# Performance work log

Measured on AMD Instinct MI355X. Metric: run time of the kernel, lower is better.

## Reference

```python
import jax, jax.numpy as jnp
import numpy as np

B, T, E, H = 4, 2048, 512, 8
D = E // H  # head_dim = 64


def setup_inputs() -> dict:
    key = jax.random.key(0)
    ks = jax.random.split(key, 9)
    s = 1.0 / np.sqrt(E)
    inp = {
        "x": jax.random.normal(ks[0], (B, T, E), dtype=jnp.float32),
        "Wq": jax.random.normal(ks[1], (E, E), dtype=jnp.float32) * s,
        "bq": jnp.zeros((E,), dtype=jnp.float32),
        "Wk": jax.random.normal(ks[2], (E, E), dtype=jnp.float32) * s,
        "bk": jnp.zeros((E,), dtype=jnp.float32),
        "Wv": jax.random.normal(ks[3], (E, E), dtype=jnp.float32) * s,
        "bv": jnp.zeros((E,), dtype=jnp.float32),
        "Wo": jax.random.normal(ks[4], (E, E), dtype=jnp.float32) * s,
        "bo": jnp.zeros((E,), dtype=jnp.float32),
    }
    return inp


def reference(x, Wq, bq, Wk, bk, Wv, bv, Wo, bo):
    # x: (B, T, E); weights stored (in, out) so y = x @ W + b
    b, t, _ = x.shape
    q = (x @ Wq + bq).reshape(b, t, H, D).transpose(0, 2, 1, 3)  # (B,H,T,D)
    k = (x @ Wk + bk).reshape(b, t, H, D).transpose(0, 2, 1, 3)  # (B,H,T,D)
    v = (x @ Wv + bv).reshape(b, t, H, D).transpose(0, 2, 1, 3)  # (B,H,T,D)
    scores = jnp.einsum("bhqd,bhkd->bhqk", q, k) / np.sqrt(D)    # (B,H,Tq,Tk)
    # faithful to source: softmax over dim=-2 (the query axis)
    attn = jax.nn.softmax(scores, axis=-2)
    out = jnp.einsum("bhqk,bhkd->bhqd", attn, v)                  # (B,H,T,D)
    # faithful to source: reshape (B,H,T,D) -> (B,T,H*D) with NO transpose
    out = out.reshape(b, t, H * D)
    return out @ Wo + bo
```

## Files before the change

### kernel.cpp

```cpp
#include <hip/hip_runtime.h>
#include <hip/hip_bf16.h>

#define NB 4
#define NT 2048
#define NE 512
#define NH 8
#define ND 64
#define BH (NB*NH)

typedef __attribute__((ext_vector_type(8))) short short8;
typedef __attribute__((ext_vector_type(4))) short short4v;
typedef __attribute__((ext_vector_type(4))) float f32x4;

typedef const __attribute__((address_space(3))) short* lds_sp;

__device__ __forceinline__ f32x4 mfma16(short8 a, short8 b, f32x4 c){
  return __builtin_amdgcn_mfma_f32_16x16x32_bf16(a, b, c, 0, 0, 0);
}
__device__ __forceinline__ short f2b(float f){
  union { float f; unsigned u; } v; v.f = f;
  unsigned r = v.u + 0x7FFFu + ((v.u >> 16) & 1u);
  return (short)(r >> 16);
}
__device__ __forceinline__ float b2f(short s){
  union { unsigned u; float f; } v; v.u = ((unsigned)(unsigned short)s) << 16; return v.f;
}
__device__ __forceinline__ unsigned pk2(float a, float b){
  union { __hip_bfloat162 h; unsigned u; } v;
  v.h = __float22bfloat162_rn(make_float2(a, b));
  return v.u;
}
__device__ __forceinline__ void gld16(const void* g, void* l){
  __builtin_amdgcn_global_load_lds((const __attribute__((address_space(1))) void*)g,
                                   (__attribute__((address_space(3))) void*)l, 16, 0, 0);
}
__device__ __forceinline__ short4v trr(lds_sp p, int imm){
  short4v r;
  asm volatile("ds_read_b64_tr_b16 %0, %1 offset:%2" : "=v"(r) : "v"(p), "i"(imm));
  return r;
}

__global__ __launch_bounds__(256) void pack_x_k(const float* __restrict__ x, short* __restrict__ xb){
  int i = blockIdx.x*256 + threadIdx.x;
  f32x4 a = ((const f32x4*)x)[2*i];
  f32x4 b = ((const f32x4*)x)[2*i+1];
  union { short8 s; unsigned u[4]; } o;
  o.u[0] = pk2(a[0], a[1]);
  o.u[1] = pk2(a[2], a[3]);
  o.u[2] = pk2(b[0], b[1]);
  o.u[3] = pk2(b[2], b[3]);
  ((short8*)xb)[i] = o.s;
}

__global__ __launch_bounds__(256) void pack_wt_k(const float* __restrict__ Wq, const float* __restrict__ Wk,
                                                 const float* __restrict__ Wv, const float* __restrict__ Wo,
                                                 short* __restrict__ Wt){
  const float* W = blockIdx.z==0?Wq: blockIdx.z==1?Wk: blockIdx.z==2?Wv:Wo;
  short* out = Wt + (size_t)blockIdx.z*NE*NE;
  __shared__ float t[32][33];
  int tx = threadIdx.x & 31, ty = threadIdx.x >> 5;
  int j0 = blockIdx.x*32, e0 = blockIdx.y*32;
#pragma unroll
  for (int r = 0; r < 4; ++r)
    t[ty*4+r][tx] = W[(size_t)(e0+ty*4+r)*NE + j0+tx];
  __syncthreads();
#pragma unroll
  for (int r = 0; r < 4; ++r)
    out[(size_t)(j0+ty*4+r)*NE + e0+tx] = f2b(t[tx][ty*4+r]);
}

__global__ __launch_bounds__(256) void gemm_qkv_k(const short* __restrict__ xb, const short* __restrict__ Wt,
                                                  const float* __restrict__ bq, const float* __restrict__ bk,
                                                  const float* __restrict__ bv,
                                                  short* __restrict__ Q, short* __restrict__ K, short* __restrict__ V){
  int z = blockIdx.z;
  const short* Bm = Wt + (size_t)z*NE*NE;
  const float* bias = z==0?bq: z==1?bk:bv;
  short* out = z==0?Q: z==1?K:V;
  float scale = (z==0) ? 0.125f : 1.0f;

  __shared__ short As[128*32];
  __shared__ short Bs[128*32];
  int tid = threadIdx.x, lane = tid & 63, wid = tid >> 6;
  int m0 = blockIdx.y*128, n0 = blockIdx.x*128;
  int wm = wid >> 1, wn = wid & 1;
  int sr = lane >> 2, sg = lane & 3;
  int fr = lane & 15, fg = lane >> 4;

  f32x4 acc[4][4] = {};

  for (int kt = 0; kt < 16; ++kt){
    int k0 = kt*32;
    {
      int ii0 = wid*2, ii1 = wid*2+1;
      int r0 = ii0*16 + sr, r1 = ii1*16 + sr;
      gld16(xb + (size_t)(m0 + r0)*NE + k0 + ((sg ^ (r0&3))<<3), (short*)As + ii0*512);
      gld16(xb + (size_t)(m0 + r1)*NE + k0 + ((sg ^ (r1&3))<<3), (short*)As + ii1*512);
      gld16(Bm + (size_t)(n0 + r0)*NE + k0 + ((sg ^ (r0&3))<<3), (short*)Bs + ii0*512);
      gld16(Bm + (size_t)(n0 + r1)*NE + k0 + ((sg ^ (r1&3))<<3), (short*)Bs + ii1*512);
    }
    __syncthreads();
    short8 af[4], bf[4];
#pragma unroll
    for (int m = 0; m < 4; ++m){
      int row = wm*64 + m*16 + fr;
      af[m] = *(const short8*)&As[row*32 + ((fg ^ (row&3))<<3)];
    }
#pragma unroll
    for (int n = 0; n < 4; ++n){
      int row = wn*64 + n*16 + fr;
      bf[n] = *(const short8*)&Bs[row*32 + ((fg ^ (row&3))<<3)];
    }
#pragma unroll
    for (int m = 0; m < 4; ++m)
#pragma unroll
      for (int n = 0; n < 4; ++n)
        acc[m][n] = mfma16(af[m], bf[n], acc[m][n]);
    __syncthreads();
  }
#pragma unroll
  for (int m = 0; m < 4; ++m)
#pragma unroll
    for (int n = 0; n < 4; ++n)
#pragma unroll
      for (int i = 0; i < 4; ++i){
        int row = m0 + wm*64 + m*16 + fg*4 + i;
        int col = n0 + wn*64 + n*16 + fr;
        float v = (acc[m][n][i] + bias[col]) * scale;
        int b = row >> 11, t = row & (NT-1), h = col >> 6, d = col & 63;
        out[(((size_t)(b*NH + h)*NT + t)<<6) + d] = f2b(v);
      }
}

__global__ __launch_bounds__(512, 4) void attn_l_k(const short* __restrict__ Q, const short* __restrict__ K,
                                                   float* __restrict__ lbuf){
  int bid = blockIdx.x;
  int bh = (bid & 7)*4 + ((bid >> 3) & 3);
  int kt = bid >> 5;
  const short* Qh = Q + (size_t)bh*NT*ND;
  const short* Kh = K + (size_t)bh*NT*ND;
  __shared__ short Qs[2][8192];
  int tid = threadIdx.x, lane = tid&63, wid = tid>>6;
  int fr = lane&15, fg = lane>>4;
  int sr = lane>>3, sg = lane&7;

  int krow = kt*128 + wid*16;
  short8 ak[2];
#pragma unroll
  for (int dh = 0; dh < 2; ++dh)
    ak[dh] = *(const short8*)&Kh[(size_t)(krow + fr)*ND + dh*32 + fg*8];

  const short* qsrc0 = Qh + (size_t)(wid*16 + sr)*ND + ((sg ^ sr)<<3);
  const short* qsrc1 = qsrc0 + 8*ND;
  auto stage = [&](int t, int bf){
    size_t adv = (size_t)t*128*ND;
    gld16(qsrc0 + adv, (short*)&Qs[bf][wid*1024]);
    gld16(qsrc1 + adv, (short*)&Qs[bf][wid*1024 + 512]);
  };
  stage(0, 0);
  __syncthreads();

  float rs[4] = {0.f,0.f,0.f,0.f};

  for (int qt = 0; qt < 16; ++qt){
    int cur = qt & 1;
    if (qt < 15) stage(qt+1, cur^1);
    const short* Qt = &Qs[cur][0];
#pragma unroll
    for (int qf = 0; qf < 8; ++qf){
      int row = qf*16 + fr;
      short8 b0 = *(const short8*)&Qt[row*64 + ((fg ^ (row&7))<<3)];
      short8 b1 = *(const short8*)&Qt[row*64 + (((4+fg) ^ (row&7))<<3)];
      f32x4 c = {};
      c = mfma16(ak[0], b0, c);
      c = mfma16(ak[1], b1, c);
#pragma unroll
      for (int i = 0; i < 4; ++i)
        rs[i] += __expf(c[i]);
    }
    __syncthreads();
  }

#pragma unroll
  for (int i = 0; i < 4; ++i){
    float v = rs[i];
    v += __shfl_xor(v, 1); v += __shfl_xor(v, 2);
    v += __shfl_xor(v, 4); v += __shfl_xor(v, 8);
    if (fr == 0) lbuf[(size_t)bh*NT + krow + fg*4 + i] = v;
  }
}

__global__ __launch_bounds__(256) void scale_v_k(const short* __restrict__ V, const float* __restrict__ lbuf,
                                                 short* __restrict__ Vp){
  int idx = blockIdx.x*256 + threadIdx.x;
  int R = idx >> 3, d0 = (idx&7)*8;
  float inv = 1.0f / lbuf[R];
  short8 v = *(const short8*)&V[((size_t)R<<6) + d0];
  union { short8 s; unsigned u[4]; } o;
#pragma unroll
  for (int j = 0; j < 4; ++j)
    o.u[j] = pk2(b2f(v[2*j])*inv, b2f(v[2*j+1])*inv);
  *(short8*)&Vp[((size_t)R<<6) + d0] = o.s;
}

__global__ __launch_bounds__(256, 3) void attn_out_k(const short* __restrict__ Q, const short* __restrict__ K,
                                                     const short* __restrict__ Vp,
                                                     short* __restrict__ out2){
  int bid = blockIdx.x;
  int xcd = bid & 7, w = bid >> 3;
  int bh = xcd*4 + (w & 3);
  int q0 = (w >> 2) * 128;
  int b = bh >> 3, h = bh & 7;
  const short* Qh = Q + (size_t)bh*NT*ND;
  const short* Kh = K + (size_t)bh*NT*ND;
  const short* Vh = Vp + (size_t)bh*NT*ND;
  __shared__ short S[2][8192];
  int tid = threadIdx.x, lane = tid&63, wid = tid>>6;
  int fr = lane&15, fg = lane>>4;
  int sr = lane>>3, sg = lane&7;
  int qw = q0 + wid*32;

  short8 qreg[2][2];
#pragma unroll
  for (int qf = 0; qf < 2; ++qf)
#pragma unroll
    for (int dh = 0; dh < 2; ++dh)
      qreg[qf][dh] = *(const short8*)&Qh[(size_t)(qw + qf*16 + fr)*ND + dh*32 + fg*8];

  const short* ksrc0 = Kh + (size_t)(wid*16 + sr)*ND + ((sg ^ sr)<<3);
  const short* ksrc1 = ksrc0 + 8*ND;
  int vt0 = wid*4 + (lane>>5);
  int vt1 = vt0 + 2;
  int vr = (lane&31)>>1, vc0 = (lane&1)*8;
  const short* vsrc0 = Vh + (size_t)((vt0>>2)*16 + vr)*ND + (vt0&3)*16 + vc0;
  const short* vsrc1 = Vh + (size_t)((vt1>>2)*16 + vr)*ND + (vt1&3)*16 + vc0;

  auto stage = [&](int t, int bf){
    size_t adv = (size_t)t*64*ND;
    gld16(ksrc0 + adv, (short*)&S[bf][wid*1024]);
    gld16(ksrc1 + adv, (short*)&S[bf][wid*1024 + 512]);
    gld16(vsrc0 + adv, (short*)&S[bf][4096 + wid*1024]);
    gld16(vsrc1 + adv, (short*)&S[bf][4096 + wid*1024 + 512]);
  };

  stage(0, 0);
  __syncthreads();

  f32x4 oacc[2][4] = {};

  for (int kt = 0; kt < 32; ++kt){
    int cur = kt & 1;
    if (kt < 31) stage(kt+1, cur^1);

    const short* Ks = &S[cur][0];

    short8 ak[4][2];
#pragma unroll
    for (int rf = 0; rf < 4; ++rf){
      int row = rf*16 + fr;
#pragma unroll
      for (int dh = 0; dh < 2; ++dh)
        ak[rf][dh] = *(const short8*)&Ks[row*64 + (((dh*4+fg) ^ (row&7))<<3)];
    }
    short8 pa[2][2];
#pragma unroll
    for (int qf = 0; qf < 2; ++qf){
      f32x4 s[4];
      __builtin_amdgcn_s_setprio(1);
#pragma unroll
      for (int rf = 0; rf < 4; ++rf){
        f32x4 c = {};
        c = mfma16(ak[rf][0], qreg[qf][0], c);
        c = mfma16(ak[rf][1], qreg[qf][1], c);
        s[rf] = c;
      }
      __builtin_amdgcn_s_setprio(0);
#pragma unroll
      for (int c = 0; c < 2; ++c){
        union { short8 s8; unsigned u[4]; } p;
        p.u[0] = pk2(__expf(s[2*c  ][0]), __expf(s[2*c  ][1]));
        p.u[1] = pk2(__expf(s[2*c  ][2]), __expf(s[2*c  ][3]));
        p.u[2] = pk2(__expf(s[2*c+1][0]), __expf(s[2*c+1][1]));
        p.u[3] = pk2(__expf(s[2*c+1][2]), __expf(s[2*c+1][3]));
        pa[qf][c] = p.s8;
      }
    }

    lds_sp vbase = (lds_sp)(const short*)((const short*)&S[cur][4096] + lane*4);
#pragma unroll
    for (int c = 0; c < 2; ++c){
      short4v t0[4], t1[4];
#pragma unroll
      for (int n = 0; n < 4; ++n){
        t0[n] = trr(vbase, ((2*c  )*4 + n)*512);
        t1[n] = trr(vbase, ((2*c+1)*4 + n)*512);
      }
      asm volatile("s_waitcnt lgkmcnt(0)");
      __builtin_amdgcn_sched_barrier(0);
      __builtin_amdgcn_s_setprio(1);
#pragma unroll
      for (int n = 0; n < 4; ++n){
        short8 vb = __builtin_shufflevector(t0[n], t1[n], 0,1,2,3,4,5,6,7);
#pragma unroll
        for (int qf = 0; qf < 2; ++qf)
          oacc[qf][n] = mfma16(pa[qf][c], vb, oacc[qf][n]);
      }
      __builtin_amdgcn_s_setprio(0);
    }
    __syncthreads();
  }

#pragma unroll
  for (int qf = 0; qf < 2; ++qf)
#pragma unroll
    for (int n = 0; n < 4; ++n)
#pragma unroll
      for (int i = 0; i < 4; ++i){
        int t = qw + qf*16 + fg*4 + i;
        int d = n*16 + fr;
        int r = h*256 + (t>>3);
        int e = ((t&7)<<6) + d;
        out2[((size_t)(b*NT + r)<<9) + e] = f2b(oacc[qf][n][i]);
      }
}

__global__ __launch_bounds__(256) void gemm_out_k(const short* __restrict__ A, const short* __restrict__ Bm,
                                                  const float* __restrict__ bo, float* __restrict__ out){
  __shared__ short As[128*32];
  __shared__ short Bs[128*32];
  int tid = threadIdx.x, lane = tid & 63, wid = tid >> 6;
  int m0 = blockIdx.y*128, n0 = blockIdx.x*128;
  int wm = wid >> 1, wn = wid & 1;
  int sr = lane >> 2, sg = lane & 3;
  int fr = lane & 15, fg = lane >> 4;

  f32x4 acc[4][4] = {};

  for (int kt = 0; kt < 16; ++kt){
    int k0 = kt*32;
    {
      int ii0 = wid*2, ii1 = wid*2+1;
      int r0 = ii0*16 + sr, r1 = ii1*16 + sr;
      gld16(A  + (size_t)(m0 + r0)*NE + k0 + ((sg ^ (r0&3))<<3), (short*)As + ii0*512);
      gld16(A  + (size_t)(m0 + r1)*NE + k0 + ((sg ^ (r1&3))<<3), (short*)As + ii1*512);
      gld16(Bm + (size_t)(n0 + r0)*NE + k0 + ((sg ^ (r0&3))<<3), (short*)Bs + ii0*512);
      gld16(Bm + (size_t)(n0 + r1)*NE + k0 + ((sg ^ (r1&3))<<3), (short*)Bs + ii1*512);
    }
    __syncthreads();
    short8 af[4], bf[4];
#pragma unroll
    for (int m = 0; m < 4; ++m){
      int row = wm*64 + m*16 + fr;
      af[m] = *(const short8*)&As[row*32 + ((fg ^ (row&3))<<3)];
    }
#pragma unroll
    for (int n = 0; n < 4; ++n){
      int row = wn*64 + n*16 + fr;
      bf[n] = *(const short8*)&Bs[row*32 + ((fg ^ (row&3))<<3)];
    }
#pragma unroll
    for (int m = 0; m < 4; ++m)
#pragma unroll
      for (int n = 0; n < 4; ++n)
        acc[m][n] = mfma16(af[m], bf[n], acc[m][n]);
    __syncthreads();
  }
#pragma unroll
  for (int m = 0; m < 4; ++m)
#pragma unroll
    for (int n = 0; n < 4; ++n)
#pragma unroll
      for (int i = 0; i < 4; ++i){
        int row = m0 + wm*64 + m*16 + fg*4 + i;
        int col = n0 + wn*64 + n*16 + fr;
        out[(size_t)row*NE + col] = acc[m][n][i] + bo[col];
      }
}

extern "C" void kernel_launch(void* const* d_in, const int* in_sizes, int n_in,
                              void* d_out, int out_size, void* d_ws, size_t ws_size,
                              hipStream_t stream){
  const float* x  = (const float*)d_in[0];
  const float* Wq = (const float*)d_in[1];
  const float* bq = (const float*)d_in[2];
  const float* Wk = (const float*)d_in[3];
  const float* bk = (const float*)d_in[4];
  const float* Wv = (const float*)d_in[5];
  const float* bv = (const float*)d_in[6];
  const float* Wo = (const float*)d_in[7];
  const float* bo = (const float*)d_in[8];
  float* out = (float*)d_out;

  char* ws = (char*)d_ws;
  size_t off = 0;
  auto alloc = [&](size_t bytes){ void* p = ws + off; off = (off + bytes + 255) & ~(size_t)255; return p; };
  short* xb    = (short*)alloc((size_t)NB*NT*NE*2);
  short* Wt    = (short*)alloc((size_t)4*NE*NE*2);
  short* Qb    = (short*)alloc((size_t)NB*NT*NE*2);
  short* Kb    = (short*)alloc((size_t)NB*NT*NE*2);
  short* Vb    = (short*)alloc((size_t)NB*NT*NE*2);
  short* Vp    = (short*)alloc((size_t)NB*NT*NE*2);
  float* lbuf  = (float*)alloc((size_t)BH*NT*sizeof(float));
  short* out2  = (short*)alloc((size_t)NB*NT*NE*2);
  (void)ws_size; (void)in_sizes; (void)n_in; (void)out_size;

  pack_x_k<<<dim3((NB*NT*NE/8)/256), dim3(256), 0, stream>>>(x, xb);
  pack_wt_k<<<dim3(NE/32, NE/32, 4), dim3(256), 0, stream>>>(Wq, Wk, Wv, Wo, Wt);
  gemm_qkv_k<<<dim3(NE/128, (NB*NT)/128, 3), dim3(256), 0, stream>>>(xb, Wt, bq, bk, bv, Qb, Kb, Vb);
  attn_l_k<<<dim3((NT/128)*BH), dim3(512), 0, stream>>>(Qb, Kb, lbuf);
  scale_v_k<<<dim3((NB*NT*NE/8)/256), dim3(256), 0, stream>>>(Vb, lbuf, Vp);
  attn_out_k<<<dim3((NT/128)*BH), dim3(256), 0, stream>>>(Qb, Kb, Vp, out2);
  gemm_out_k<<<dim3(NE/128, (NB*NT)/128), dim3(256), 0, stream>>>(out2, Wt + (size_t)3*NE*NE, bo, out);
}
```

Measured before the change: 118.5 us.

## Halve attention query tile per block and fold log2e into Q scale for exp2

The attention-output kernel now gives each wave 16 query rows instead of 32, so each block covers 64 queries, twice as many blocks launch, and the occupancy hint rises from 3 to 4 blocks per CU. The Q projection scale now includes log2(e), so the softmax kernels can call exp2f directly instead of __expf. The smaller tile cuts register pressure and adds parallelism. In exchange, K/V tiles are reloaded from global memory by twice as many blocks, which halves the reuse of each staged tile.

```diff
diff --git a/kernel.cpp b/kernel.cpp
--- a/kernel.cpp
+++ b/kernel.cpp
@@ -7,6 +7,8 @@
 #define NH 8
 #define ND 64
 #define BH (NB*NH)
+
+#define LOG2E 1.44269504088896340736f
 
 typedef __attribute__((ext_vector_type(8))) short short8;
 typedef __attribute__((ext_vector_type(4))) short short4v;
@@ -77,7 +79,7 @@
   const short* Bm = Wt + (size_t)z*NE*NE;
   const float* bias = z==0?bq: z==1?bk:bv;
   short* out = z==0?Q: z==1?K:V;
-  float scale = (z==0) ? 0.125f : 1.0f;
+  float scale = (z==0) ? 0.125f*LOG2E : 1.0f;
 
   __shared__ short As[128*32];
   __shared__ short Bs[128*32];
@@ -176,7 +178,7 @@
       c = mfma16(ak[1], b1, c);
 #pragma unroll
       for (int i = 0; i < 4; ++i)
-        rs[i] += __expf(c[i]);
+        rs[i] += exp2f(c[i]);
     }
     __syncthreads();
   }
@@ -203,13 +205,13 @@
   *(short8*)&Vp[((size_t)R<<6) + d0] = o.s;
 }
 
-__global__ __launch_bounds__(256, 3) void attn_out_k(const short* __restrict__ Q, const short* __restrict__ K,
+__global__ __launch_bounds__(256, 4) void attn_out_k(const short* __restrict__ Q, const short* __restrict__ K,
                                                      const short* __restrict__ Vp,
                                                      short* __restrict__ out2){
   int bid = blockIdx.x;
   int xcd = bid & 7, w = bid >> 3;
   int bh = xcd*4 + (w & 3);
-  int q0 = (w >> 2) * 128;
+  int q0 = (w >> 2) * 64;
   int b = bh >> 3, h = bh & 7;
   const short* Qh = Q + (size_t)bh*NT*ND;
   const short* Kh = K + (size_t)bh*NT*ND;
@@ -218,14 +220,12 @@
   int tid = threadIdx.x, lane = tid&63, wid = tid>>6;
   int fr = lane&15, fg = lane>>4;
   int sr = lane>>3, sg = lane&7;
-  int qw = q0 + wid*32;
-
-  short8 qreg[2][2];
-#pragma unroll
-  for (int qf = 0; qf < 2; ++qf)
-#pragma unroll
-    for (int dh = 0; dh < 2; ++dh)
-      qreg[qf][dh] = *(const short8*)&Qh[(size_t)(qw + qf*16 + fr)*ND + dh*32 + fg*8];
+  int qw = q0 + wid*16;
+
+  short8 qreg[2];
+#pragma unroll
+  for (int dh = 0; dh < 2; ++dh)
+    qreg[dh] = *(const short8*)&Qh[(size_t)(qw + fr)*ND + dh*32 + fg*8];
 
   const short* ksrc0 = Kh + (size_t)(wid*16 + sr)*ND + ((sg ^ sr)<<3);
   const short* ksrc1 = ksrc0 + 8*ND;
@@ -246,7 +246,7 @@
   stage(0, 0);
   __syncthreads();
 
-  f32x4 oacc[2][4] = {};
+  f32x4 oacc[4] = {};
 
   for (int kt = 0; kt < 32; ++kt){
     int cur = kt & 1;
@@ -262,28 +262,25 @@
       for (int dh = 0; dh < 2; ++dh)
         ak[rf][dh] = *(const short8*)&Ks[row*64 + (((dh*4+fg) ^ (row&7))<<3)];
     }
-    short8 pa[2][2];
-#pragma unroll
-    for (int qf = 0; qf < 2; ++qf){
-      f32x4 s[4];
-      __builtin_amdgcn_s_setprio(1);
-#pragma unroll
-      for (int rf = 0; rf < 4; ++rf){
-        f32x4 c = {};
-        c = mfma16(ak[rf][0], qreg[qf][0], c);
-        c = mfma16(ak[rf][1], qreg[qf][1], c);
-        s[rf] = c;
-      }
-      __builtin_amdgcn_s_setprio(0);
-#pragma unroll
-      for (int c = 0; c < 2; ++c){
-        union { short8 s8; unsigned u[4]; } p;
-        p.u[0] = pk2(__expf(s[2*c  ][0]), __expf(s[2*c  ][1]));
-        p.u[1] = pk2(__expf(s[2*c  ][2]), __expf(s[2*c  ][3]));
-        p.u[2] = pk2(__expf(s[2*c+1][0]), __expf(s[2*c+1][1]));
-        p.u[3] = pk2(__expf(s[2*c+1][2]), __expf(s[2*c+1][3]));
-        pa[qf][c] = p.s8;
-      }
+    f32x4 s[4];
+    __builtin_amdgcn_s_setprio(1);
+#pragma unroll
+    for (int rf = 0; rf < 4; ++rf){
+      f32x4 c = {};
+      c = mfma16(ak[rf][0], qreg[0], c);
+      c = mfma16(ak[rf][1], qreg[1], c);
+      s[rf] = c;
+    }
+    __builtin_amdgcn_s_setprio(0);
+    short8 pa[2];
+#pragma unroll
+    for (int c = 0; c < 2; ++c){
+      union { short8 s8; unsigned u[4]; } p;
+      p.u[0] = pk2(exp2f(s[2*c  ][0]), exp2f(s[2*c  ][1]));
+      p.u[1] = pk2(exp2f(s[2*c  ][2]), exp2f(s[2*c  ][3]));
+      p.u[2] = pk2(exp2f(s[2*c+1][0]), exp2f(s[2*c+1][1]));
+      p.u[3] = pk2(exp2f(s[2*c+1][2]), exp2f(s[2*c+1][3]));
+      pa[c] = p.s8;
     }
 
     lds_sp vbase = (lds_sp)(const short*)((const short*)&S[cur][4096] + lane*4);
@@ -301,9 +298,7 @@
 #pragma unroll
       for (int n = 0; n < 4; ++n){
         short8 vb = __builtin_shufflevector(t0[n], t1[n], 0,1,2,3,4,5,6,7);
-#pragma unroll
-        for (int qf = 0; qf < 2; ++qf)
-          oacc[qf][n] = mfma16(pa[qf][c], vb, oacc[qf][n]);
+        oacc[n] = mfma16(pa[c], vb, oacc[n]);
       }
       __builtin_amdgcn_s_setprio(0);
     }
@@ -311,17 +306,15 @@
   }
 
 #pragma unroll
-  for (int qf = 0; qf < 2; ++qf)
-#pragma unroll
-    for (int n = 0; n < 4; ++n)
-#pragma unroll
-      for (int i = 0; i < 4; ++i){
-        int t = qw + qf*16 + fg*4 + i;
-        int d = n*16 + fr;
-        int r = h*256 + (t>>3);
-        int e = ((t&7)<<6) + d;
-        out2[((size_t)(b*NT + r)<<9) + e] = f2b(oacc[qf][n][i]);
-      }
+  for (int n = 0; n < 4; ++n)
+#pragma unroll
+    for (int i = 0; i < 4; ++i){
+      int t = qw + fg*4 + i;
+      int d = n*16 + fr;
+      int r = h*256 + (t>>3);
+      int e = ((t&7)<<6) + d;
+      out2[((size_t)(b*NT + r)<<9) + e] = f2b(oacc[n][i]);
+    }
 }
 
 __global__ __launch_bounds__(256) void gemm_out_k(const short* __restrict__ A, const short* __restrict__ Bm,
@@ -409,6 +402,6 @@
   gemm_qkv_k<<<dim3(NE/128, (NB*NT)/128, 3), dim3(256), 0, stream>>>(xb, Wt, bq, bk, bv, Qb, Kb, Vb);
   attn_l_k<<<dim3((NT/128)*BH), dim3(512), 0, stream>>>(Qb, Kb, lbuf);
   scale_v_k<<<dim3((NB*NT*NE/8)/256), dim3(256), 0, stream>>>(Vb, lbuf, Vp);
-  attn_out_k<<<dim3((NT/128)*BH), dim3(256), 0, stream>>>(Qb, Kb, Vp, out2);
+  attn_out_k<<<dim3((NT/64)*BH), dim3(256), 0, stream>>>(Qb, Kb, Vp, out2);
   gemm_out_k<<<dim3(NE/128, (NB*NT)/128), dim3(256), 0, stream>>>(out2, Wt + (size_t)3*NE*NE, bo, out);
 }
```

Result: slower. 143.6 us (+21.2%).

## Triple-buffer K/V staging in attention and fold log2e into Q scale for exp2

Applied to the files above, without the earlier changes.

The attention kernel's K/V LDS staging goes from double to triple buffering. Loads are now issued two tiles ahead, and the kernel waits with a partial vmcnt plus a single barrier per iteration instead of two __syncthreads. Separately, log2(e) is folded into the Q projection scale so that __expf can become exp2f in both the row-sum and output kernels. The aim is to hide global load latency and shave the multiply inside exp. The price is 50% more LDS per block, which may reduce occupancy. The clamped redundant final loads also rely on vmcnt counting being correct.

```diff
diff --git a/kernel.cpp b/kernel.cpp
--- a/kernel.cpp
+++ b/kernel.cpp
@@ -7,6 +7,8 @@
 #define NH 8
 #define ND 64
 #define BH (NB*NH)
+
+#define LOG2E 1.44269504088896340736f
 
 typedef __attribute__((ext_vector_type(8))) short short8;
 typedef __attribute__((ext_vector_type(4))) short short4v;
@@ -77,7 +79,7 @@
   const short* Bm = Wt + (size_t)z*NE*NE;
   const float* bias = z==0?bq: z==1?bk:bv;
   short* out = z==0?Q: z==1?K:V;
-  float scale = (z==0) ? 0.125f : 1.0f;
+  float scale = (z==0) ? 0.125f*LOG2E : 1.0f;
 
   __shared__ short As[128*32];
   __shared__ short Bs[128*32];
@@ -176,7 +178,7 @@
       c = mfma16(ak[1], b1, c);
 #pragma unroll
       for (int i = 0; i < 4; ++i)
-        rs[i] += __expf(c[i]);
+        rs[i] += exp2f(c[i]);
     }
     __syncthreads();
   }
@@ -214,7 +216,7 @@
   const short* Qh = Q + (size_t)bh*NT*ND;
   const short* Kh = K + (size_t)bh*NT*ND;
   const short* Vh = Vp + (size_t)bh*NT*ND;
-  __shared__ short S[2][8192];
+  __shared__ short S[3][8192];
   int tid = threadIdx.x, lane = tid&63, wid = tid>>6;
   int fr = lane&15, fg = lane>>4;
   int sr = lane>>3, sg = lane&7;
@@ -244,15 +246,23 @@
   };
 
   stage(0, 0);
-  __syncthreads();
+  stage(1, 1);
 
   f32x4 oacc[2][4] = {};
+  int bcur = 0;
 
   for (int kt = 0; kt < 32; ++kt){
-    int cur = kt & 1;
-    if (kt < 31) stage(kt+1, cur^1);
-
-    const short* Ks = &S[cur][0];
+    asm volatile("s_waitcnt vmcnt(4)" ::: "memory");
+    __builtin_amdgcn_s_barrier();
+    __builtin_amdgcn_sched_barrier(0);
+
+    {
+      int t2 = kt + 2 <= 31 ? kt + 2 : 31;
+      int bnx = bcur + 2; if (bnx >= 3) bnx -= 3;
+      stage(t2, bnx);
+    }
+
+    const short* Ks = &S[0][0] + bcur*8192;
 
     short8 ak[4][2];
 #pragma unroll
@@ -278,15 +288,15 @@
 #pragma unroll
       for (int c = 0; c < 2; ++c){
         union { short8 s8; unsigned u[4]; } p;
-        p.u[0] = pk2(__expf(s[2*c  ][0]), __expf(s[2*c  ][1]));
-        p.u[1] = pk2(__expf(s[2*c  ][2]), __expf(s[2*c  ][3]));
-        p.u[2] = pk2(__expf(s[2*c+1][0]), __expf(s[2*c+1][1]));
-        p.u[3] = pk2(__expf(s[2*c+1][2]), __expf(s[2*c+1][3]));
+        p.u[0] = pk2(exp2f(s[2*c  ][0]), exp2f(s[2*c  ][1]));
+        p.u[1] = pk2(exp2f(s[2*c  ][2]), exp2f(s[2*c  ][3]));
+        p.u[2] = pk2(exp2f(s[2*c+1][0]), exp2f(s[2*c+1][1]));
+        p.u[3] = pk2(exp2f(s[2*c+1][2]), exp2f(s[2*c+1][3]));
         pa[qf][c] = p.s8;
       }
     }
 
-    lds_sp vbase = (lds_sp)(const short*)((const short*)&S[cur][4096] + lane*4);
+    lds_sp vbase = (lds_sp)(const short*)(&S[0][0] + bcur*8192 + 4096 + lane*4);
 #pragma unroll
     for (int c = 0; c < 2; ++c){
       short4v t0[4], t1[4];
@@ -307,7 +317,7 @@
       }
       __builtin_amdgcn_s_setprio(0);
     }
-    __syncthreads();
+    bcur = bcur + 1 == 3 ? 0 : bcur + 1;
   }
 
 #pragma unroll
```

After: 143.1 us. +20.8%, slower.
